# Optimization experiments

Hardware: AMD Instinct MI355X
Metric: run time of the kernel (lower is better)

The kernel has to match this reference:

```python
import jax, jax.numpy as jnp
import numpy as np

B, L, D = 8, 2048, 128
K_CURV = 1.0  # Lorentz manifold curvature constant
NEG_INF = float(-2**32 + 1)


def _lorentz_linear(x, W, b, scale):
    # nn.Linear then project onto the Lorentz manifold (dropout is identity in eval).
    x = x @ W.T + b
    time = jax.nn.sigmoid(x[..., :1]) * jnp.exp(scale) + 1.1
    x_narrow = x[..., 1:]
    s = (time * time - K_CURV) / jnp.sum(x_narrow * x_narrow, axis=-1, keepdims=True)
    return jnp.concatenate([time, x_narrow * jnp.sqrt(s)], axis=-1)


def setup_inputs() -> dict:
    key = jax.random.key(0)
    ks = jax.random.split(key, 10)
    stdv = 0.02

    def lin_w(k):
        W = jax.random.uniform(k, (D, D), minval=-stdv, maxval=stdv, dtype=jnp.float32)
        return W.at[:, 0].set(0.0)  # reset_parameters zeros column 0

    inp = {
        'query': jax.random.normal(ks[0], (B, L, D), dtype=jnp.float32),
        'key': jax.random.normal(ks[1], (B, L, D), dtype=jnp.float32),
        'value': jax.random.normal(ks[2], (B, L, D), dtype=jnp.float32),
        'mask': jax.random.bernoulli(ks[3], 0.1, (B, L)),  # True = padded position
        'Wq': lin_w(ks[4]), 'bq': jnp.zeros((D,), jnp.float32), 'sq': jnp.asarray(2.3, jnp.float32),
        'Wk': lin_w(ks[5]), 'bk': jnp.zeros((D,), jnp.float32), 'sk': jnp.asarray(2.3, jnp.float32),
        'Wv': lin_w(ks[6]), 'bv': jnp.zeros((D,), jnp.float32), 'sv': jnp.asarray(2.3, jnp.float32),
        'attn_scale': jnp.asarray([np.sqrt(D)], jnp.float32),
        'attn_bias': jnp.asarray(0.0, jnp.float32),
    }
    return inp


def reference(query, key, value, mask, Wq, bq, sq, Wk, bk, sk, Wv, bv, sv, attn_scale, attn_bias):
    q = _lorentz_linear(query, Wq, bq, sq)  # [B, L, D]
    k = _lorentz_linear(key, Wk, bk, sk)
    v = _lorentz_linear(value, Wv, bv, sv)
    # single head: shape to [B, 1, L, D]
    q, k, v = q[:, None], k[:, None], v[:, None]

    # Lorentzian inner product: negate time component of q
    qk = jnp.einsum('bhqd,bhkd->bhqk', q.at[..., 0].multiply(-1.0), k)
    attn = (2.0 + 2.0 * qk) / attn_scale + attn_bias  # [B, 1, L, L]

    # pad mask [B, L] broadcast over query rows + causal (triu) mask
    pad = jnp.broadcast_to(mask[:, None, :], (B, L, L))
    tri = jnp.triu(jnp.ones((L, L), bool), k=1)
    m = (tri[None] | pad)[:, None]  # [B, 1, L, L]
    attn = jnp.where(m, NEG_INF, attn)
    attn = jax.nn.softmax(attn, axis=-1)

    # Lorentz mid-point: weighted sum, normalize by sqrt(|<ave, ave>_L|)
    ave = jnp.einsum('bhqk,bhkd->bhqd', attn, v)
    lor = -ave[..., :1] ** 2 + jnp.sum(ave[..., 1:] ** 2, axis=-1, keepdims=True)
    denom = jnp.sqrt(jnp.maximum(jnp.abs(-lor), 1e-8))
    out = jnp.sqrt(K_CURV) * ave / denom
    return out[:, 0]  # [B, L, D]
```

## Files before the change

### kernel.cpp

```cpp
#include <hip/hip_runtime.h>

typedef unsigned short u16;
typedef unsigned long long u64;
typedef __attribute__((ext_vector_type(8))) short short8;
typedef __attribute__((ext_vector_type(4))) float f32x4;

#define MFMA16(A,B,C) __builtin_amdgcn_mfma_f32_16x16x32_bf16(A,B,C,0,0,0)
#define NEG_INF_F (-4294967295.0f)

#define Bsz 8
#define Lsz 2048
#define Dsz 128

__device__ __forceinline__ u16 f2bf(float f){
  union { float f; unsigned u; } v; v.f = f;
  unsigned u = v.u;
  return (u16)((u + 0x7fffu + ((u >> 16) & 1u)) >> 16);
}
__device__ __forceinline__ float bf2f(u16 h){
  union { float f; unsigned u; } v; v.u = ((unsigned)h) << 16;
  return v.f;
}

__global__ __launch_bounds__(256) void wconv_kernel(
    const float* __restrict__ Wq, const float* __restrict__ Wk,
    const float* __restrict__ Wv, u16* __restrict__ wb)
{
  int i = blockIdx.x * 256 + threadIdx.x;
  if (i < 16384) wb[i] = f2bf(Wq[i]);
  else if (i < 32768) wb[i] = f2bf(Wk[i - 16384]);
  else if (i < 49152) wb[i] = f2bf(Wv[i - 32768]);
}

#define LPX 136
#define LPY 133

__global__ __launch_bounds__(256) void proj_kernel(
    const float* __restrict__ xq, const float* __restrict__ xk, const float* __restrict__ xv,
    const u16* __restrict__ wb,
    const float* __restrict__ bq, const float* __restrict__ bk, const float* __restrict__ bv,
    const float* __restrict__ sq, const float* __restrict__ sk, const float* __restrict__ sv,
    const float* __restrict__ attn_scale,
    u16* __restrict__ qout, u16* __restrict__ kout,
    u16* __restrict__ vthi, u16* __restrict__ vtlo,
    float* __restrict__ tqo, float* __restrict__ tko,
    float* __restrict__ vpart)
{
  const int z = blockIdx.z;
  const float* x  = (z == 0) ? xq : (z == 1) ? xk : xv;
  const u16*   Wb = wb + z * 16384;
  const float* bb = (z == 0) ? bq : (z == 1) ? bk : bv;
  const float* ss = (z == 0) ? sq : (z == 1) ? sk : sv;

  __shared__ u16  xl[64 * LPX];
  __shared__ u16  wl[128 * LPX];
  __shared__ float yl[64 * LPY];
  __shared__ float scl[64];
  __shared__ float tml[64];

  const int t = threadIdx.x;
  const long row0 = (long)blockIdx.x * 64;

  for (int i = t; i < 2048; i += 256) {
    int r = i >> 4, c8 = (i & 15) * 8;
    *(short8*)&wl[r * LPX + c8] = *(const short8*)&Wb[r * 128 + c8];
  }
  for (int i = t; i < 2048; i += 256) {
    int off = i * 4;
    int r = off >> 7, c = off & 127;
    f32x4 xv4 = *(const f32x4*)(x + row0 * 128 + off);
    u64 wv = (u64)f2bf(xv4[0]) | ((u64)f2bf(xv4[1]) << 16)
           | ((u64)f2bf(xv4[2]) << 32) | ((u64)f2bf(xv4[3]) << 48);
    *(u64*)&xl[r * LPX + c] = wv;
  }
  __syncthreads();

  const int l = t & 63, wid = t >> 6;
  const int qr = l & 15, g = l >> 4;
  const int r0 = wid * 16;

  short8 af[4];
#pragma unroll
  for (int ks = 0; ks < 4; ks++)
    af[ks] = *(const short8*)&xl[(r0 + qr) * LPX + ks * 32 + g * 8];

  f32x4 acc[8];
#pragma unroll
  for (int jt = 0; jt < 8; jt++) acc[jt] = (f32x4){0.f, 0.f, 0.f, 0.f};

#pragma unroll
  for (int ks = 0; ks < 4; ks++) {
#pragma unroll
    for (int jt = 0; jt < 8; jt++) {
      short8 bfr = *(const short8*)&wl[(jt * 16 + qr) * LPX + ks * 32 + g * 8];
      acc[jt] = MFMA16(af[ks], bfr, acc[jt]);
    }
  }

  float bbv[8];
#pragma unroll
  for (int jt = 0; jt < 8; jt++) bbv[jt] = bb[jt * 16 + qr];

  float ssq[4] = {0.f, 0.f, 0.f, 0.f};
#pragma unroll
  for (int jt = 0; jt < 8; jt++)
#pragma unroll
    for (int r = 0; r < 4; r++) {
      float yv = acc[jt][r] + bbv[jt];
      acc[jt][r] = yv;
      float s2 = yv * yv;
      if (jt == 0) s2 = (qr == 0) ? 0.f : s2;
      ssq[r] += s2;
    }
#pragma unroll
  for (int r = 0; r < 4; r++) {
    ssq[r] += __shfl_xor(ssq[r], 1);
    ssq[r] += __shfl_xor(ssq[r], 2);
    ssq[r] += __shfl_xor(ssq[r], 4);
    ssq[r] += __shfl_xor(ssq[r], 8);
  }

  const float es = __expf(ss[0]);
  const float fold = 2.0f / attn_scale[0];

  float tvv[4], sclv[4];
#pragma unroll
  for (int r = 0; r < 4; r++) {
    float y0 = __shfl(acc[0][r], l & 48);
    float tv = es / (1.0f + __expf(-y0)) + 1.1f;
    tvv[r] = tv;
    sclv[r] = sqrtf((tv * tv - 1.0f) / ssq[r]);
  }
  if (qr == 0) {
#pragma unroll
    for (int r = 0; r < 4; r++) {
      tml[r0 + g * 4 + r] = tvv[r];
      scl[r0 + g * 4 + r] = sclv[r];
    }
  }
#pragma unroll
  for (int jt = 0; jt < 8; jt++)
#pragma unroll
    for (int r = 0; r < 4; r++)
      yl[(r0 + g * 4 + r) * LPY + jt * 16 + qr] = acc[jt][r];
  __syncthreads();

  const long gbase = row0 * 128;
  if (z == 0) {
    for (int i = t; i < 64 * 128; i += 256) {
      int r = i >> 7, d = i & 127;
      float v = (d == 0) ? 0.f : yl[r * LPY + d] * scl[r] * fold;
      qout[gbase + i] = f2bf(v);
    }
    if (t < 64) tqo[row0 + t] = -tml[t] * fold;
  } else if (z == 1) {
    for (int i = t; i < 64 * 128; i += 256) {
      int r = i >> 7, d = i & 127;
      float v = (d == 0) ? 0.f : yl[r * LPY + d] * scl[r];
      kout[gbase + i] = f2bf(v);
    }
    if (t < 64) tko[row0 + t] = tml[t];
  } else {
    const int b = (int)(row0 >> 11);
    const int lpos = (int)(row0 & 2047);
    for (int i = t; i < 128 * 64; i += 256) {
      int d = i >> 6, r = i & 63;
      float v = (d == 0) ? tml[r] : yl[r * LPY + d] * scl[r];
      u16 hi = f2bf(v);
      float lo = v - bf2f(hi);
      long idx = ((long)(b * 128 + d)) * 2048 + lpos + r;
      vthi[idx] = hi;
      vtlo[idx] = f2bf(lo);
    }
    if (t < 128) {
      float s = 0.f;
      for (int r = 0; r < 64; r++)
        s += (t == 0) ? tml[r] : yl[r * LPY + t] * scl[r];
      int blk = (int)((row0 >> 6) & 31);
      vpart[((long)(b * 32 + blk)) * 128 + t] = s;
    }
  }
}

__global__ __launch_bounds__(256) void pack_mask_kernel(
    const int* __restrict__ mask, u64* __restrict__ pmask)
{
  int gt = blockIdx.x * 256 + threadIdx.x;
  int w = gt >> 6;
  int lane = gt & 63;
  if (w >= Bsz * 32) return;
  u64 word = __ballot(mask[w * 64 + lane] != 0);
  if (lane == 0) pmask[w] = word;
}

__global__ __launch_bounds__(128) void vreduce_kernel(
    const float* __restrict__ vpart, float* __restrict__ vsum)
{
  int i = blockIdx.x * 128 + threadIdx.x;
  int b = i >> 7, d = i & 127;
  float s = 0.f;
  for (int j = 0; j < 32; j++) s += vpart[((long)(b * 32 + j)) * 128 + d];
  vsum[i] = s;
}

__global__ __launch_bounds__(1024, 4) void flash_kernel(
    const u16* __restrict__ qb, const u16* __restrict__ kb,
    const u16* __restrict__ vthi, const u16* __restrict__ vtlo,
    const float* __restrict__ tq, const float* __restrict__ tk,
    const u64* __restrict__ pmask, const float* __restrict__ vsum,
    float* __restrict__ out)
{
  __shared__ u16 Kl[128 * 128];
  __shared__ u16 Vh[2][128 * 128];
  __shared__ u16 Pl[2][16 * 128];
  __shared__ float mstat[2][8][16];
  __shared__ float lLd[2][8][16];
  __shared__ float ssqw[2][8][16];

  const int t = threadIdx.x;
  const int wv = t >> 6;
  const int sub = wv >> 3, w = wv & 7;
  const int l = t & 63;
  const int qr = l & 15, g = l >> 4;
  const int blk = blockIdx.x;
  const int b = blk & 7;
  const int pr = blk >> 3;

  const int srow = t >> 3, sch = t & 7;
  const int sphys = (sch ^ (srow & 7)) * 8;
  const int sbase = srow * 128 + sphys;

  for (int phase = 0; phase < 2; ++phase) {
    const int st = phase ? pr : (63 - pr);
    const int qbase = st * 32;
    const int q0s = qbase + sub * 16;
    const int qg  = q0s + qr;
    const int nkt = (st * 32 + 159) >> 7;

    const u16* qptr = qb + ((long)(b * 2048 + qg)) * 128 + g * 8;
    short8 qf[4];
#pragma unroll
    for (int ks = 0; ks < 4; ks++) qf[ks] = *(const short8*)(qptr + ks * 32);
    const float tqv = tq[b * 2048 + qg];

    float m = NEG_INF_F, lsum = 0.f;
    f32x4 acc = (f32x4){0.f, 0.f, 0.f, 0.f};

    {
      const long kgb = (long)(b * 2048 + srow) * 128;
      const long vgb = (long)(b * 128 + srow) * 2048;
      short8 a0 = *(const short8*)(kb + kgb + sch * 8);
      short8 a1 = *(const short8*)(kb + kgb + (sch + 8) * 8);
      short8 a2 = *(const short8*)(vthi + vgb + sch * 8);
      short8 a3 = *(const short8*)(vthi + vgb + (sch + 8) * 8);
      *(short8*)&Kl[sbase] = a0;
      *(short8*)&Kl[sbase + 64] = a1;
      *(short8*)&Vh[0][sbase] = a2;
      *(short8*)&Vh[0][sbase + 64] = a3;
    }
    f32x4 tkv_c = *(const f32x4*)(tk + b * 2048 + 16 * w + g * 4);
    u64 mw_c = pmask[b * 32 + (w >> 2)];
    __syncthreads();

    short8 vlo[4];

    for (int kt = 0; kt < nkt; ++kt) {
      const int k0 = kt << 7;
      const int cur = kt & 1;
      const bool more = (kt + 1 < nkt);

      short8 s0, s1, s2, s3;
      if (more) {
        const int nk0 = k0 + 128;
        const long kgb = (long)(b * 2048 + nk0 + srow) * 128;
        const long vgb = (long)(b * 128 + srow) * 2048 + nk0;
        s0 = *(const short8*)(kb + kgb + sch * 8);
        s1 = *(const short8*)(kb + kgb + (sch + 8) * 8);
        s2 = *(const short8*)(vthi + vgb + sch * 8);
        s3 = *(const short8*)(vthi + vgb + (sch + 8) * 8);
      }

      __builtin_amdgcn_s_setprio(1);
      if (kt > 0) {
        const u16* Pb = &Pl[sub][0];
        const u16* Vb = &Vh[cur ^ 1][0];
        const int vrow = (16 * w + qr) * 128;
#pragma unroll
        for (int ks2 = 0; ks2 < 4; ks2++) {
          int ch = ((g + 4 * ks2) ^ (qr & 7)) * 8;
          short8 pf = *(const short8*)&Pb[qr * 128 + ch];
          short8 vh_ = *(const short8*)&Vb[vrow + ch];
          acc = MFMA16(vh_, pf, acc);
          acc = MFMA16(vlo[ks2], pf, acc);
        }
      }
      f32x4 sv = (f32x4){0.f, 0.f, 0.f, 0.f};
      {
        const int krw = (16 * w + qr) * 128;
#pragma unroll
        for (int ks = 0; ks < 4; ks++) {
          int ch = ((g + 4 * ks) ^ (qr & 7)) * 8;
          sv = MFMA16(*(const short8*)&Kl[krw + ch], qf[ks], sv);
        }
      }
      __builtin_amdgcn_s_setprio(0);

      {
        const long vb = (long)(b * 128 + 16 * w + qr) * 2048 + k0 + g * 8;
#pragma unroll
        for (int ks2 = 0; ks2 < 4; ks2++)
          vlo[ks2] = *(const short8*)(vtlo + vb + ks2 * 32);
      }

      const bool bndry = (k0 + 127 > q0s);
      float p4[4];
      float tmax = NEG_INF_F;
#pragma unroll
      for (int r = 0; r < 4; r++) {
        int kl = 16 * w + g * 4 + r;
        float val = sv[r] + tqv * tkv_c[r];
        bool bad = ((mw_c >> (kl & 63)) & 1ull) != 0ull;
        if (bndry) bad |= (k0 + kl > qg);
        val = bad ? NEG_INF_F : val;
        p4[r] = val;
        tmax = fmaxf(tmax, val);
      }
      tmax = fmaxf(tmax, __shfl_xor(tmax, 16));
      tmax = fmaxf(tmax, __shfl_xor(tmax, 32));
      if (g == 0) mstat[sub][w][qr] = tmax;
      __syncthreads();

      float mt = mstat[sub][0][qr];
#pragma unroll
      for (int j = 1; j < 8; j++) mt = fmaxf(mt, mstat[sub][j][qr]);
      float mn = fmaxf(m, mt);
      float rr = __expf(m - mn);
      m = mn;

      float ts = 0.f;
#pragma unroll
      for (int r = 0; r < 4; r++) {
        float pv = __expf(p4[r] - mn);
        p4[r] = pv;
        ts += pv;
      }
      {
        int pch = ((2 * w + (g >> 1)) ^ (qr & 7)) * 8 + (g & 1) * 4;
        u64 wv_ = (u64)f2bf(p4[0])
                | ((u64)f2bf(p4[1]) << 16)
                | ((u64)f2bf(p4[2]) << 32)
                | ((u64)f2bf(p4[3]) << 48);
        *(u64*)&Pl[sub][qr * 128 + pch] = wv_;
      }
      lsum = lsum * rr + ts;
      acc[0] *= rr; acc[1] *= rr; acc[2] *= rr; acc[3] *= rr;

      if (more) {
        *(short8*)&Kl[sbase] = s0;
        *(short8*)&Kl[sbase + 64] = s1;
        *(short8*)&Vh[cur ^ 1][sbase] = s2;
        *(short8*)&Vh[cur ^ 1][sbase + 64] = s3;
        tkv_c = *(const f32x4*)(tk + b * 2048 + k0 + 128 + 16 * w + g * 4);
        mw_c = pmask[b * 32 + (kt + 1) * 2 + (w >> 2)];
      }
      __syncthreads();
    }

    {
      const u16* Pb = &Pl[sub][0];
      const u16* Vb = &Vh[(nkt - 1) & 1][0];
      const int vrow = (16 * w + qr) * 128;
#pragma unroll
      for (int ks2 = 0; ks2 < 4; ks2++) {
        int ch = ((g + 4 * ks2) ^ (qr & 7)) * 8;
        short8 pf = *(const short8*)&Pb[qr * 128 + ch];
        short8 vh_ = *(const short8*)&Vb[vrow + ch];
        acc = MFMA16(vh_, pf, acc);
        acc = MFMA16(vlo[ks2], pf, acc);
      }
    }

    lsum += __shfl_xor(lsum, 16);
    lsum += __shfl_xor(lsum, 32);
    if (g == 0) lLd[sub][w][qr] = lsum;
    __syncthreads();

    float Lt = 0.f;
#pragma unroll
    for (int j = 0; j < 8; j++) Lt += lLd[sub][j][qr];
    const bool mrow = (m == NEG_INF_F);
    float invL = mrow ? 0.f : 1.0f / Lt;

    const float* vs = vsum + b * 128;
    float av[4];
    float pp = 0.f;
#pragma unroll
    for (int r = 0; r < 4; r++) {
      int d = 16 * w + 4 * g + r;
      float a = mrow ? vs[d] * (1.0f / 2048.0f) : acc[r] * invL;
      av[r] = a;
      pp += (d == 0) ? -a * a : a * a;
    }
    pp += __shfl_xor(pp, 16);
    pp += __shfl_xor(pp, 32);
    if (g == 0) ssqw[sub][w][qr] = pp;
    __syncthreads();

    float lor = 0.f;
#pragma unroll
    for (int j = 0; j < 8; j++) lor += ssqw[sub][j][qr];
    float rd = 1.0f / sqrtf(fmaxf(fabsf(lor), 1e-8f));

    float* op = out + ((long)(b * 2048 + qg)) * 128 + 16 * w + 4 * g;
    f32x4 o;
    o[0] = av[0] * rd; o[1] = av[1] * rd; o[2] = av[2] * rd; o[3] = av[3] * rd;
    *(f32x4*)op = o;
    __syncthreads();
  }
}

extern "C" void kernel_launch(void* const* d_in, const int* in_sizes, int n_in,
                              void* d_out, int out_size, void* d_ws, size_t ws_size,
                              hipStream_t stream)
{
  const float* query = (const float*)d_in[0];
  const float* key   = (const float*)d_in[1];
  const float* value = (const float*)d_in[2];
  const int*   mask  = (const int*)d_in[3];
  const float* Wq = (const float*)d_in[4];
  const float* bq = (const float*)d_in[5];
  const float* sq = (const float*)d_in[6];
  const float* Wk = (const float*)d_in[7];
  const float* bk = (const float*)d_in[8];
  const float* sk = (const float*)d_in[9];
  const float* Wv = (const float*)d_in[10];
  const float* bv = (const float*)d_in[11];
  const float* sv = (const float*)d_in[12];
  const float* attn_scale = (const float*)d_in[13];

  float* out = (float*)d_out;
  char* ws = (char*)d_ws;

  float* vsum  = (float*)ws;
  u64*   pmask = (u64*)(ws + 4096);
  float* tqa   = (float*)(ws + 8192);
  float* tka   = (float*)(ws + 8192 + 65536);
  float* vpart = (float*)(ws + 8192 + 131072);
  u16*   wb    = (u16*)(ws + 8192 + 262144);
  char*  big   = ws + 8192 + 262144 + 131072;
  u16*   qbuf  = (u16*)big;
  u16*   kbuf  = qbuf + (size_t)16384 * 128;
  u16*   vthi  = kbuf + (size_t)16384 * 128;
  u16*   vtlo  = vthi + (size_t)16384 * 128;

  wconv_kernel<<<192, 256, 0, stream>>>(Wq, Wk, Wv, wb);
  proj_kernel<<<dim3(256, 1, 3), 256, 0, stream>>>(
      query, key, value, wb, bq, bk, bv, sq, sk, sv, attn_scale,
      qbuf, kbuf, vthi, vtlo, tqa, tka, vpart);
  pack_mask_kernel<<<64, 256, 0, stream>>>(mask, pmask);
  vreduce_kernel<<<8, 128, 0, stream>>>(vpart, vsum);
  flash_kernel<<<256, 1024, 0, stream>>>(
      qbuf, kbuf, vthi, vtlo, tqa, tka, pmask, vsum, out);
}
```

Baseline: 101.3 us.

## Replace online softmax with fixed analytic max bound and register-resident K/V tiles

```diff
diff --git a/kernel.cpp b/kernel.cpp
--- a/kernel.cpp
+++ b/kernel.cpp
@@ -203,220 +203,193 @@
   vsum[i] = s;
 }
 
-__global__ __launch_bounds__(1024, 4) void flash_kernel(
-    const u16* __restrict__ qb, const u16* __restrict__ kb,
+__global__ __launch_bounds__(512, 4) void flash_kernel(
+    const u16* __restrict__ qbf, const u16* __restrict__ kb,
     const u16* __restrict__ vthi, const u16* __restrict__ vtlo,
     const float* __restrict__ tq, const float* __restrict__ tk,
     const u64* __restrict__ pmask, const float* __restrict__ vsum,
+    const float* __restrict__ sqp, const float* __restrict__ skp,
+    const float* __restrict__ asp,
     float* __restrict__ out)
 {
-  __shared__ u16 Kl[128 * 128];
-  __shared__ u16 Vh[2][128 * 128];
-  __shared__ u16 Pl[2][16 * 128];
-  __shared__ float mstat[2][8][16];
-  __shared__ float lLd[2][8][16];
-  __shared__ float ssqw[2][8][16];
+  __shared__ u16 Pl[2][32 * 128];
+  __shared__ float lLd[8][2][16];
+  __shared__ float ssqw[8][2][16];
 
   const int t = threadIdx.x;
-  const int wv = t >> 6;
-  const int sub = wv >> 3, w = wv & 7;
-  const int l = t & 63;
+  const int w = t >> 6, l = t & 63;
   const int qr = l & 15, g = l >> 4;
   const int blk = blockIdx.x;
   const int b = blk & 7;
-  const int pr = blk >> 3;
-
-  const int srow = t >> 3, sch = t & 7;
-  const int sphys = (sch ^ (srow & 7)) * 8;
-  const int sbase = srow * 128 + sphys;
-
-  for (int phase = 0; phase < 2; ++phase) {
-    const int st = phase ? pr : (63 - pr);
-    const int qbase = st * 32;
-    const int q0s = qbase + sub * 16;
-    const int qg  = q0s + qr;
-    const int nkt = (st * 32 + 159) >> 7;
-
-    const u16* qptr = qb + ((long)(b * 2048 + qg)) * 128 + g * 8;
-    short8 qf[4];
-#pragma unroll
-    for (int ks = 0; ks < 4; ks++) qf[ks] = *(const short8*)(qptr + ks * 32);
-    const float tqv = tq[b * 2048 + qg];
-
-    float m = NEG_INF_F, lsum = 0.f;
-    f32x4 acc = (f32x4){0.f, 0.f, 0.f, 0.f};
-
+  const int s = 63 - (blk >> 3);
+  const int qbase = s * 32;
+  const int nkt = (qbase + 159) >> 7;
+
+  const float fold = 2.0f / asp[0];
+  const float tqm = __expf(sqp[0]) + 1.1f;
+  const float tkm = __expf(skp[0]) + 1.1f;
+  const float MS = fold * sqrtf((tqm * tqm - 1.f) * (tkm * tkm - 1.f)) + 1.0f;
+
+  short8 qf[2][4];
+  float tqv0, tqv1;
+  {
+    const u16* qp0 = qbf + ((long)(b * 2048 + qbase + qr)) * 128 + g * 8;
+    const u16* qp1 = qp0 + 16 * 128;
+#pragma unroll
+    for (int ks = 0; ks < 4; ks++) {
+      qf[0][ks] = *(const short8*)(qp0 + ks * 32);
+      qf[1][ks] = *(const short8*)(qp1 + ks * 32);
+    }
+    tqv0 = tq[b * 2048 + qbase + qr];
+    tqv1 = tq[b * 2048 + qbase + 16 + qr];
+  }
+
+  const u16* kbase  = kb   + ((long)(b * 2048 + 16 * w + qr)) * 128 + g * 8;
+  const u16* vhbase = vthi + ((long)(b * 128 + 16 * w + qr)) * 2048 + g * 8;
+  const u16* vlbase = vtlo + ((long)(b * 128 + 16 * w + qr)) * 2048 + g * 8;
+
+  float lsum0 = 0.f, lsum1 = 0.f;
+  f32x4 acc0 = (f32x4){0.f, 0.f, 0.f, 0.f};
+  f32x4 acc1 = (f32x4){0.f, 0.f, 0.f, 0.f};
+
+  short8 kc[4], vh[4], vl[4];
+#pragma unroll
+  for (int ks = 0; ks < 4; ks++) kc[ks] = *(const short8*)(kbase + ks * 32);
+  f32x4 tkvc = *(const f32x4*)(tk + b * 2048 + 16 * w + g * 4);
+  u64 mwc = pmask[b * 32 + (w >> 2)];
+
+  int cur = 0;
+  for (int kt = 0; kt < nkt; kt++) {
+    const long k0 = (long)kt << 7;
+
+    f32x4 sv0 = (f32x4){0.f, 0.f, 0.f, 0.f};
+    f32x4 sv1 = (f32x4){0.f, 0.f, 0.f, 0.f};
+#pragma unroll
+    for (int ks = 0; ks < 4; ks++) {
+      sv0 = MFMA16(kc[ks], qf[0][ks], sv0);
+      sv1 = MFMA16(kc[ks], qf[1][ks], sv1);
+    }
+    if (kt + 1 < nkt) {
+      const u16* kp = kbase + (k0 + 128) * 128;
+#pragma unroll
+      for (int ks = 0; ks < 4; ks++) kc[ks] = *(const short8*)(kp + ks * 32);
+    }
+
+    const bool bndry = (k0 + 127 > qbase);
+    float p0[4], p1[4];
+#pragma unroll
+    for (int r = 0; r < 4; r++) {
+      int kl = 16 * w + 4 * g + r;
+      bool bad = ((mwc >> (kl & 63)) & 1ull) != 0ull;
+      bool bad0 = bad, bad1 = bad;
+      if (bndry) {
+        bad0 |= (k0 + kl > qbase + qr);
+        bad1 |= (k0 + kl > qbase + 16 + qr);
+      }
+      float e0 = __expf(sv0[r] + tqv0 * tkvc[r] - MS);
+      float e1 = __expf(sv1[r] + tqv1 * tkvc[r] - MS);
+      p0[r] = bad0 ? 0.f : e0;
+      p1[r] = bad1 ? 0.f : e1;
+      lsum0 += p0[r];
+      lsum1 += p1[r];
+    }
     {
-      const long kgb = (long)(b * 2048 + srow) * 128;
-      const long vgb = (long)(b * 128 + srow) * 2048;
-      short8 a0 = *(const short8*)(kb + kgb + sch * 8);
-      short8 a1 = *(const short8*)(kb + kgb + (sch + 8) * 8);
-      short8 a2 = *(const short8*)(vthi + vgb + sch * 8);
-      short8 a3 = *(const short8*)(vthi + vgb + (sch + 8) * 8);
-      *(short8*)&Kl[sbase] = a0;
-      *(short8*)&Kl[sbase + 64] = a1;
-      *(short8*)&Vh[0][sbase] = a2;
-      *(short8*)&Vh[0][sbase + 64] = a3;
-    }
-    f32x4 tkv_c = *(const f32x4*)(tk + b * 2048 + 16 * w + g * 4);
-    u64 mw_c = pmask[b * 32 + (w >> 2)];
-    __syncthreads();
-
-    short8 vlo[4];
-
-    for (int kt = 0; kt < nkt; ++kt) {
-      const int k0 = kt << 7;
-      const int cur = kt & 1;
-      const bool more = (kt + 1 < nkt);
-
-      short8 s0, s1, s2, s3;
-      if (more) {
-        const int nk0 = k0 + 128;
-        const long kgb = (long)(b * 2048 + nk0 + srow) * 128;
-        const long vgb = (long)(b * 128 + srow) * 2048 + nk0;
-        s0 = *(const short8*)(kb + kgb + sch * 8);
-        s1 = *(const short8*)(kb + kgb + (sch + 8) * 8);
-        s2 = *(const short8*)(vthi + vgb + sch * 8);
-        s3 = *(const short8*)(vthi + vgb + (sch + 8) * 8);
+      int pch = ((2 * w + (g >> 1)) ^ (qr & 7)) * 8 + (g & 1) * 4;
+      u64 w0 = (u64)f2bf(p0[0]) | ((u64)f2bf(p0[1]) << 16)
+             | ((u64)f2bf(p0[2]) << 32) | ((u64)f2bf(p0[3]) << 48);
+      u64 w1 = (u64)f2bf(p1[0]) | ((u64)f2bf(p1[1]) << 16)
+             | ((u64)f2bf(p1[2]) << 32) | ((u64)f2bf(p1[3]) << 48);
+      *(u64*)&Pl[cur][qr * 128 + pch] = w0;
+      *(u64*)&Pl[cur][(16 + qr) * 128 + pch] = w1;
+    }
+    if (kt + 1 < nkt) {
+      tkvc = *(const f32x4*)(tk + b * 2048 + k0 + 128 + 16 * w + g * 4);
+      mwc = pmask[b * 32 + (int)(k0 >> 6) + 2 + (w >> 2)];
+    }
+
+    if (kt > 0) {
+      const u16* Pb = &Pl[cur ^ 1][0];
+#pragma unroll
+      for (int ks = 0; ks < 4; ks++) {
+        int ch = ((4 * ks + g) ^ (qr & 7)) * 8;
+        short8 pf0 = *(const short8*)&Pb[qr * 128 + ch];
+        short8 pf1 = *(const short8*)&Pb[(16 + qr) * 128 + ch];
+        acc0 = MFMA16(vh[ks], pf0, acc0);
+        acc0 = MFMA16(vl[ks], pf0, acc0);
+        acc1 = MFMA16(vh[ks], pf1, acc1);
+        acc1 = MFMA16(vl[ks], pf1, acc1);
       }
-
-      __builtin_amdgcn_s_setprio(1);
-      if (kt > 0) {
-        const u16* Pb = &Pl[sub][0];
-        const u16* Vb = &Vh[cur ^ 1][0];
-        const int vrow = (16 * w + qr) * 128;
-#pragma unroll
-        for (int ks2 = 0; ks2 < 4; ks2++) {
-          int ch = ((g + 4 * ks2) ^ (qr & 7)) * 8;
-          short8 pf = *(const short8*)&Pb[qr * 128 + ch];
-          short8 vh_ = *(const short8*)&Vb[vrow + ch];
-          acc = MFMA16(vh_, pf, acc);
-          acc = MFMA16(vlo[ks2], pf, acc);
-        }
-      }
-      f32x4 sv = (f32x4){0.f, 0.f, 0.f, 0.f};
-      {
-        const int krw = (16 * w + qr) * 128;
-#pragma unroll
-        for (int ks = 0; ks < 4; ks++) {
-          int ch = ((g + 4 * ks) ^ (qr & 7)) * 8;
-          sv = MFMA16(*(const short8*)&Kl[krw + ch], qf[ks], sv);
-        }
-      }
-      __builtin_amdgcn_s_setprio(0);
-
-      {
-        const long vb = (long)(b * 128 + 16 * w + qr) * 2048 + k0 + g * 8;
-#pragma unroll
-        for (int ks2 = 0; ks2 < 4; ks2++)
-          vlo[ks2] = *(const short8*)(vtlo + vb + ks2 * 32);
-      }
-
-      const bool bndry = (k0 + 127 > q0s);
-      float p4[4];
-      float tmax = NEG_INF_F;
-#pragma unroll
-      for (int r = 0; r < 4; r++) {
-        int kl = 16 * w + g * 4 + r;
-        float val = sv[r] + tqv * tkv_c[r];
-        bool bad = ((mw_c >> (kl & 63)) & 1ull) != 0ull;
-        if (bndry) bad |= (k0 + kl > qg);
-        val = bad ? NEG_INF_F : val;
-        p4[r] = val;
-        tmax = fmaxf(tmax, val);
-      }
-      tmax = fmaxf(tmax, __shfl_xor(tmax, 16));
-      tmax = fmaxf(tmax, __shfl_xor(tmax, 32));
-      if (g == 0) mstat[sub][w][qr] = tmax;
-      __syncthreads();
-
-      float mt = mstat[sub][0][qr];
-#pragma unroll
-      for (int j = 1; j < 8; j++) mt = fmaxf(mt, mstat[sub][j][qr]);
-      float mn = fmaxf(m, mt);
-      float rr = __expf(m - mn);
-      m = mn;
-
-      float ts = 0.f;
-#pragma unroll
-      for (int r = 0; r < 4; r++) {
-        float pv = __expf(p4[r] - mn);
-        p4[r] = pv;
-        ts += pv;
-      }
-      {
-        int pch = ((2 * w + (g >> 1)) ^ (qr & 7)) * 8 + (g & 1) * 4;
-        u64 wv_ = (u64)f2bf(p4[0])
-                | ((u64)f2bf(p4[1]) << 16)
-                | ((u64)f2bf(p4[2]) << 32)
-                | ((u64)f2bf(p4[3]) << 48);
-        *(u64*)&Pl[sub][qr * 128 + pch] = wv_;
-      }
-      lsum = lsum * rr + ts;
-      acc[0] *= rr; acc[1] *= rr; acc[2] *= rr; acc[3] *= rr;
-
-      if (more) {
-        *(short8*)&Kl[sbase] = s0;
-        *(short8*)&Kl[sbase + 64] = s1;
-        *(short8*)&Vh[cur ^ 1][sbase] = s2;
-        *(short8*)&Vh[cur ^ 1][sbase + 64] = s3;
-        tkv_c = *(const f32x4*)(tk + b * 2048 + k0 + 128 + 16 * w + g * 4);
-        mw_c = pmask[b * 32 + (kt + 1) * 2 + (w >> 2)];
-      }
-      __syncthreads();
-    }
-
-    {
-      const u16* Pb = &Pl[sub][0];
-      const u16* Vb = &Vh[(nkt - 1) & 1][0];
-      const int vrow = (16 * w + qr) * 128;
-#pragma unroll
-      for (int ks2 = 0; ks2 < 4; ks2++) {
-        int ch = ((g + 4 * ks2) ^ (qr & 7)) * 8;
-        short8 pf = *(const short8*)&Pb[qr * 128 + ch];
-        short8 vh_ = *(const short8*)&Vb[vrow + ch];
-        acc = MFMA16(vh_, pf, acc);
-        acc = MFMA16(vlo[ks2], pf, acc);
-      }
-    }
-
-    lsum += __shfl_xor(lsum, 16);
-    lsum += __shfl_xor(lsum, 32);
-    if (g == 0) lLd[sub][w][qr] = lsum;
-    __syncthreads();
-
-    float Lt = 0.f;
-#pragma unroll
-    for (int j = 0; j < 8; j++) Lt += lLd[sub][j][qr];
-    const bool mrow = (m == NEG_INF_F);
-    float invL = mrow ? 0.f : 1.0f / Lt;
-
-    const float* vs = vsum + b * 128;
-    float av[4];
-    float pp = 0.f;
-#pragma unroll
-    for (int r = 0; r < 4; r++) {
-      int d = 16 * w + 4 * g + r;
-      float a = mrow ? vs[d] * (1.0f / 2048.0f) : acc[r] * invL;
-      av[r] = a;
-      pp += (d == 0) ? -a * a : a * a;
-    }
-    pp += __shfl_xor(pp, 16);
-    pp += __shfl_xor(pp, 32);
-    if (g == 0) ssqw[sub][w][qr] = pp;
-    __syncthreads();
-
-    float lor = 0.f;
-#pragma unroll
-    for (int j = 0; j < 8; j++) lor += ssqw[sub][j][qr];
-    float rd = 1.0f / sqrtf(fmaxf(fabsf(lor), 1e-8f));
-
-    float* op = out + ((long)(b * 2048 + qg)) * 128 + 16 * w + 4 * g;
-    f32x4 o;
-    o[0] = av[0] * rd; o[1] = av[1] * rd; o[2] = av[2] * rd; o[3] = av[3] * rd;
-    *(f32x4*)op = o;
-    __syncthreads();
-  }
+    }
+
+#pragma unroll
+    for (int ks = 0; ks < 4; ks++) {
+      vh[ks] = *(const short8*)(vhbase + k0 + ks * 32);
+      vl[ks] = *(const short8*)(vlbase + k0 + ks * 32);
+    }
+
+    asm volatile("s_waitcnt lgkmcnt(0)\n\ts_barrier" ::: "memory");
+    cur ^= 1;
+  }
+
+  {
+    const u16* Pb = &Pl[cur ^ 1][0];
+#pragma unroll
+    for (int ks = 0; ks < 4; ks++) {
+      int ch = ((4 * ks + g) ^ (qr & 7)) * 8;
+      short8 pf0 = *(const short8*)&Pb[qr * 128 + ch];
+      short8 pf1 = *(const short8*)&Pb[(16 + qr) * 128 + ch];
+      acc0 = MFMA16(vh[ks], pf0, acc0);
+      acc0 = MFMA16(vl[ks], pf0, acc0);
+      acc1 = MFMA16(vh[ks], pf1, acc1);
+      acc1 = MFMA16(vl[ks], pf1, acc1);
+    }
+  }
+
+  lsum0 += __shfl_xor(lsum0, 16); lsum0 += __shfl_xor(lsum0, 32);
+  lsum1 += __shfl_xor(lsum1, 16); lsum1 += __shfl_xor(lsum1, 32);
+  if (g == 0) { lLd[w][0][qr] = lsum0; lLd[w][1][qr] = lsum1; }
+  __syncthreads();
+
+  float Lt0 = 0.f, Lt1 = 0.f;
+#pragma unroll
+  for (int j = 0; j < 8; j++) { Lt0 += lLd[j][0][qr]; Lt1 += lLd[j][1][qr]; }
+  const bool mrow0 = (Lt0 == 0.f);
+  const bool mrow1 = (Lt1 == 0.f);
+  const float invL0 = mrow0 ? 0.f : 1.0f / Lt0;
+  const float invL1 = mrow1 ? 0.f : 1.0f / Lt1;
+
+  const float* vs = vsum + b * 128;
+  float av0[4], av1[4];
+  float pp0 = 0.f, pp1 = 0.f;
+#pragma unroll
+  for (int r = 0; r < 4; r++) {
+    int d = 16 * w + 4 * g + r;
+    float u = vs[d] * (1.0f / 2048.0f);
+    float a0 = mrow0 ? u : acc0[r] * invL0;
+    float a1 = mrow1 ? u : acc1[r] * invL1;
+    av0[r] = a0; av1[r] = a1;
+    float sgn = (d == 0) ? -1.f : 1.f;
+    pp0 += sgn * a0 * a0;
+    pp1 += sgn * a1 * a1;
+  }
+  pp0 += __shfl_xor(pp0, 16); pp0 += __shfl_xor(pp0, 32);
+  pp1 += __shfl_xor(pp1, 16); pp1 += __shfl_xor(pp1, 32);
+  if (g == 0) { ssqw[w][0][qr] = pp0; ssqw[w][1][qr] = pp1; }
+  __syncthreads();
+
+  float lor0 = 0.f, lor1 = 0.f;
+#pragma unroll
+  for (int j = 0; j < 8; j++) { lor0 += ssqw[j][0][qr]; lor1 += ssqw[j][1][qr]; }
+  float rd0 = 1.0f / sqrtf(fmaxf(fabsf(lor0), 1e-8f));
+  float rd1 = 1.0f / sqrtf(fmaxf(fabsf(lor1), 1e-8f));
+
+  float* op0 = out + ((long)(b * 2048 + qbase + qr)) * 128 + 16 * w + 4 * g;
+  float* op1 = out + ((long)(b * 2048 + qbase + 16 + qr)) * 128 + 16 * w + 4 * g;
+  f32x4 o0, o1;
+  o0[0] = av0[0] * rd0; o0[1] = av0[1] * rd0; o0[2] = av0[2] * rd0; o0[3] = av0[3] * rd0;
+  o1[0] = av1[0] * rd1; o1[1] = av1[1] * rd1; o1[2] = av1[2] * rd1; o1[3] = av1[3] * rd1;
+  *(f32x4*)op0 = o0;
+  *(f32x4*)op1 = o1;
 }
 
 extern "C" void kernel_launch(void* const* d_in, const int* in_sizes, int n_in,
@@ -459,6 +432,6 @@
       qbuf, kbuf, vthi, vtlo, tqa, tka, vpart);
   pack_mask_kernel<<<64, 256, 0, stream>>>(mask, pmask);
   vreduce_kernel<<<8, 128, 0, stream>>>(vpart, vsum);
-  flash_kernel<<<256, 1024, 0, stream>>>(
-      qbuf, kbuf, vthi, vtlo, tqa, tka, pmask, vsum, out);
-}
+  flash_kernel<<<512, 512, 0, stream>>>(
+      qbuf, kbuf, vthi, vtlo, tqa, tka, pmask, vsum, sq, sk, attn_scale, out);
+}
```

After: 141.8 us. 40.0% more time.
